# Performance work log

Measured on AMD Instinct MI355X. Metric: run time of the kernel, lower is better.

The kernel has to match this reference:

```python
import jax, jax.numpy as jnp
import numpy as np

N_NODES = 100000
N_EDGES = 1600000
IN_DIM, HID_DIM, OUT_DIM = 128, 64, 64


def setup_inputs() -> dict:
    key = jax.random.key(0)
    ks = jax.random.split(key, 8)
    x = jax.random.normal(ks[0], (N_NODES, IN_DIM), dtype=jnp.float32)
    edge_index = jax.random.randint(ks[1], (2, N_EDGES), 0, N_NODES, dtype=jnp.int32)
    edge_weight = jax.random.uniform(ks[2], (N_EDGES,), dtype=jnp.float32)
    # GCNConv parameters (glorot-ish init)
    w1 = jax.random.normal(ks[3], (IN_DIM, HID_DIM), dtype=jnp.float32) / np.sqrt(IN_DIM)
    b1 = jnp.zeros((HID_DIM,), dtype=jnp.float32)
    w2 = jax.random.normal(ks[4], (HID_DIM, OUT_DIM), dtype=jnp.float32) / np.sqrt(HID_DIM)
    b2 = jnp.zeros((OUT_DIM,), dtype=jnp.float32)
    return {"x": x, "edge_index": edge_index, "edge_weight": edge_weight,
            "w1": w1, "b1": b1, "w2": w2, "b2": b2}


def _gcn_conv(h, src, dst, edge_weight, w, b, n_nodes):
    # GCNConv(normalize=False): linear transform, then edge-weighted scatter-add
    # (source_to_target flow: gather from src, scatter-sum into dst), then bias.
    h = h @ w                                   # [N, out]
    msg = h[src] * edge_weight[:, None]          # [E, out] irregular gather
    agg = jax.ops.segment_sum(msg, dst, num_segments=n_nodes)  # [N, out]
    return agg + b


def reference(x, edge_index, edge_weight, w1, b1, w2, b2):
    src, dst = edge_index[0], edge_index[1]
    n = x.shape[0]
    # Dropout is identity in eval mode (training=False).
    h = _gcn_conv(x, src, dst, edge_weight, w1, b1, n)
    h = jax.nn.relu(h)
    out = _gcn_conv(h, src, dst, edge_weight, w2, b2, n)
    return out
```

## Files before the change

### kernel.cpp

```cpp
#include <hip/hip_runtime.h>
#include <hip/hip_bf16.h>


#define N_NODES 100000
#define N_EDGES 1600000
#define NB1     391
#define T1      3072
#define NT1     521
#define CAP1    4706
#define GB1     782

typedef unsigned short ushort_t;
typedef unsigned int uint_t;
typedef __attribute__((ext_vector_type(8))) short bf16x8;
typedef __attribute__((ext_vector_type(4))) float floatx4;
typedef __attribute__((ext_vector_type(8))) ushort_t ushort8v;

static __device__ __forceinline__ float bf2f(ushort_t h) {
    return __uint_as_float(((uint_t)h) << 16);
}
static __device__ __forceinline__ ushort_t f2bf(float f) {
    uint_t u = __float_as_uint(f);
    u = (u + 0x7FFF + ((u >> 16) & 1)) >> 16;
    return (ushort_t)u;
}

__global__ __launch_bounds__(512) void k_init(int* __restrict__ gcursor)
{
    int t = threadIdx.x;
    if (t < NB1) gcursor[t] = t * CAP1;
}

__global__ __launch_bounds__(512) void k_p1g1(
    const int* __restrict__ src, const int* __restrict__ dst,
    const float* __restrict__ ew, int* __restrict__ gcursor,
    int2* __restrict__ recs1, int E,
    const float* __restrict__ X, const float* __restrict__ W,
    ushort_t* __restrict__ Y, int N)
{
    __shared__ __align__(16) char smem[37056];
    const int tid = threadIdx.x;

    if (blockIdx.x < NT1) {
        int* cnt     = (int*)smem;
        int* start   = cnt + NB1;
        int* cursor  = start + NB1;
        int* gb      = cursor + NB1;
        int* wsum    = (int*)(smem + 6256);
        int* wexc    = wsum + 8;
        int2* stg    = (int2*)(smem + 6336);
        ushort_t* sb = (ushort_t*)(smem + 30912);
        const int t = tid, b = blockIdx.x;
        const int lane = t & 63, wv = t >> 6;

        if (t < NB1) cnt[t] = 0;
        __syncthreads();
        const int e0 = b * T1;
        const int e1 = min(E, e0 + T1);
        for (int e = e0 + t; e < e1; e += 512)
            atomicAdd(&cnt[dst[e] >> 8], 1);
        __syncthreads();

        const int v = (t < NB1) ? cnt[t] : 0;
        int x = v;
        #pragma unroll
        for (int off = 1; off < 64; off <<= 1) {
            int y = __shfl_up(x, off);
            if (lane >= off) x += y;
        }
        if (lane == 63) wsum[wv] = x;
        __syncthreads();
        if (t < 8) {
            int w  = wsum[t];
            int xx = w;
            #pragma unroll
            for (int off = 1; off < 8; off <<= 1) {
                int y = __shfl_up(xx, off);
                if (t >= off) xx += y;
            }
            wexc[t] = xx - w;
        }
        __syncthreads();
        if (t < NB1) {
            int st = x + wexc[wv] - v;
            start[t]  = st;
            cursor[t] = st;
            gb[t]     = atomicAdd(&gcursor[t], v);
        }
        __syncthreads();

        for (int e = e0 + t; e < e1; e += 512) {
            int d  = dst[e];
            int bk = d >> 8;
            int p  = atomicAdd(&cursor[bk], 1);
            int2 r;
            r.x = ((d & 255) << 17) | src[e];
            r.y = __float_as_int(ew[e]);
            stg[p] = r;
            sb[p]  = (ushort_t)bk;
        }
        __syncthreads();
        const int n = e1 - e0;
        for (int i = t; i < n; i += 512) {
            int bk = sb[i];
            recs1[gb[bk] + (i - start[bk])] = stg[i];
        }
    } else {
        ushort_t* sA = (ushort_t*)smem;
        ushort_t* sB = (ushort_t*)(smem + 18432);
        const int b    = blockIdx.x - NT1;
        const int row0 = b * 128;

        for (int i = tid; i < 128 * 16; i += 512) {
            int k = i >> 4, n4 = (i & 15) * 4;
            float4 v = *(const float4*)(W + (size_t)k * 64 + n4);
            sB[(n4 + 0) * 136 + k] = f2bf(v.x);
            sB[(n4 + 1) * 136 + k] = f2bf(v.y);
            sB[(n4 + 2) * 136 + k] = f2bf(v.z);
            sB[(n4 + 3) * 136 + k] = f2bf(v.w);
        }
        for (int i = tid; i < 128 * 16; i += 512) {
            int r = i >> 4, c4 = (i & 15) * 4;
            int rg = row0 + r; if (rg > N - 1) rg = N - 1;
            float4 v = *(const float4*)(X + (size_t)rg * 128 + c4);
            *(ushort4*)(sA + r * 72 + c4) =
                make_ushort4(f2bf(v.x), f2bf(v.y), f2bf(v.z), f2bf(v.w));
        }
        __syncthreads();

        const int wid = tid >> 6, lane = tid & 63;
        const int m = lane & 15, quad = lane >> 4;
        floatx4 acc[4] = {};

        #pragma unroll
        for (int ksl = 0; ksl < 2; ++ksl) {
            bf16x8 a = *(const bf16x8*)(sA + (wid * 16 + m) * 72 + ksl * 32 + quad * 8);
            #pragma unroll
            for (int nt = 0; nt < 4; ++nt) {
                bf16x8 bfr = *(const bf16x8*)(sB + (nt * 16 + m) * 136 + ksl * 32 + quad * 8);
                acc[nt] = __builtin_amdgcn_mfma_f32_16x16x32_bf16(a, bfr, acc[nt], 0, 0, 0);
            }
        }
        __syncthreads();
        for (int i = tid; i < 128 * 16; i += 512) {
            int r = i >> 4, c4 = (i & 15) * 4;
            int rg = row0 + r; if (rg > N - 1) rg = N - 1;
            float4 v = *(const float4*)(X + (size_t)rg * 128 + 64 + c4);
            *(ushort4*)(sA + r * 72 + c4) =
                make_ushort4(f2bf(v.x), f2bf(v.y), f2bf(v.z), f2bf(v.w));
        }
        __syncthreads();
        #pragma unroll
        for (int ksl = 0; ksl < 2; ++ksl) {
            bf16x8 a = *(const bf16x8*)(sA + (wid * 16 + m) * 72 + ksl * 32 + quad * 8);
            #pragma unroll
            for (int nt = 0; nt < 4; ++nt) {
                bf16x8 bfr = *(const bf16x8*)(sB + (nt * 16 + m) * 136 + 64 + ksl * 32 + quad * 8);
                acc[nt] = __builtin_amdgcn_mfma_f32_16x16x32_bf16(a, bfr, acc[nt], 0, 0, 0);
            }
        }
        __syncthreads();
        #pragma unroll
        for (int nt = 0; nt < 4; ++nt)
            #pragma unroll
            for (int r = 0; r < 4; ++r)
                sA[(wid * 16 + quad * 4 + r) * 72 + nt * 16 + m] = f2bf(acc[nt][r]);
        __syncthreads();
        for (int i = tid; i < 128 * 8; i += 512) {
            int rr = i >> 3, c8 = (i & 7) * 8;
            int rg = row0 + rr;
            if (rg < N)
                *(ushort8v*)(Y + (size_t)rg * 64 + c8) =
                    *(const ushort8v*)(sA + rr * 72 + c8);
        }
    }
}

__global__ __launch_bounds__(1024) void k_pass2(
    const int2* __restrict__ recs1, const int* __restrict__ gcursor,
    int2* __restrict__ recs2, int2* __restrict__ nodeinfo, int N)
{
    __shared__ int cnt[256];
    __shared__ int s[256];
    __shared__ int cursor[256];
    const int t = threadIdx.x, b = blockIdx.x;
    const int lo = b * CAP1;
    const int hi = gcursor[b];

    if (t < 256) cnt[t] = 0;
    __syncthreads();
    for (int j = lo + t; j < hi; j += 1024)
        atomicAdd(&cnt[((uint_t)recs1[j].x) >> 17], 1);
    __syncthreads();
    const int v = (t < 256) ? cnt[t] : 0;
    if (t < 256) s[t] = v;
    #pragma unroll
    for (int off = 1; off < 256; off <<= 1) {
        __syncthreads();
        int a = (t >= off && t < 256) ? s[t - off] : 0;
        __syncthreads();
        if (t < 256) s[t] += a;
    }
    __syncthreads();
    if (t < 256) {
        const int stl = s[t] - v;
        cursor[t] = stl;
        const int ng = b * 256 + t;
        if (ng < N) {
            int2 ni; ni.x = lo + stl; ni.y = v;
            nodeinfo[ng] = ni;
        }
    }
    __syncthreads();
    for (int j = lo + t; j < hi; j += 1024) {
        int2 r = recs1[j];
        int dl = ((uint_t)r.x) >> 17;
        int p  = atomicAdd(&cursor[dl], 1);
        int2 o;
        o.x = r.x & 0x1FFFF;
        o.y = r.y;
        recs2[lo + p] = o;
    }
}

__global__ __launch_bounds__(256) void k_gemm2(
    const ushort_t* __restrict__ X, const float* __restrict__ W,
    ushort_t* __restrict__ Y, int N)
{
    __shared__ ushort_t sA[64 * 72];
    __shared__ ushort_t sB[64 * 72];
    const int tid  = threadIdx.x;
    const int row0 = blockIdx.x * 64;

    for (int i = tid; i < 64 * 16; i += 256) {
        int r = i >> 4, c4 = (i & 15) * 4;
        int rg = row0 + r; if (rg > N - 1) rg = N - 1;
        *(ushort4*)(sA + r * 72 + c4) =
            *(const ushort4*)(X + (size_t)rg * 64 + c4);
    }
    for (int i = tid; i < 64 * 16; i += 256) {
        int k = i >> 4, n4 = (i & 15) * 4;
        float4 v = *(const float4*)(W + (size_t)k * 64 + n4);
        sB[(n4 + 0) * 72 + k] = f2bf(v.x);
        sB[(n4 + 1) * 72 + k] = f2bf(v.y);
        sB[(n4 + 2) * 72 + k] = f2bf(v.z);
        sB[(n4 + 3) * 72 + k] = f2bf(v.w);
    }
    __syncthreads();

    const int wid = tid >> 6, lane = tid & 63;
    const int m = lane & 15, quad = lane >> 4;
    floatx4 acc[4] = {};

    #pragma unroll
    for (int ks = 0; ks < 2; ++ks) {
        bf16x8 a = *(const bf16x8*)(sA + (wid * 16 + m) * 72 + ks * 32 + quad * 8);
        #pragma unroll
        for (int nt = 0; nt < 4; ++nt) {
            bf16x8 bfr = *(const bf16x8*)(sB + (nt * 16 + m) * 72 + ks * 32 + quad * 8);
            acc[nt] = __builtin_amdgcn_mfma_f32_16x16x32_bf16(a, bfr, acc[nt], 0, 0, 0);
        }
    }
    __syncthreads();
    #pragma unroll
    for (int nt = 0; nt < 4; ++nt)
        #pragma unroll
        for (int r = 0; r < 4; ++r)
            sA[(wid * 16 + quad * 4 + r) * 72 + nt * 16 + m] = f2bf(acc[nt][r]);
    __syncthreads();
    for (int i = tid; i < 64 * 8; i += 256) {
        int rr = i >> 3, c8 = (i & 7) * 8;
        int rg = row0 + rr;
        if (rg < N)
            *(ushort8v*)(Y + (size_t)rg * 64 + c8) =
                *(const ushort8v*)(sA + rr * 72 + c8);
    }
}

template<bool RELU, bool OUT_BF16>
__global__ __launch_bounds__(256) void k_gather(
    const ushort_t* __restrict__ H, const int2* __restrict__ recs,
    const int2* __restrict__ nodeinfo, const float* __restrict__ bias,
    void* __restrict__ out)
{
    const int wid  = threadIdx.x >> 6;
    const int lane = threadIdx.x & 63;
    const int n0   = (blockIdx.x * 4 + wid) * 2;
    const int n1   = n0 + 1;

    const int2 niA = nodeinfo[n0];
    const int2 niB = nodeinfo[n1];
    int baseA = niA.x; const int endA = niA.x + niA.y;
    int baseB = niB.x; const int endB = niB.x + niB.y;

    const int g  = lane >> 4;
    const int c4 = (lane & 15) * 4;

    float a0 = 0.f, a1 = 0.f, a2 = 0.f, a3 = 0.f;
    float b0 = 0.f, b1 = 0.f, b2 = 0.f, b3 = 0.f;

    while (baseA < endA || baseB < endB) {
        int mA = endA - baseA; if (mA > 64) mA = 64;
        int mB = endB - baseB; if (mB > 64) mB = 64;
        int2 rA = (mA > 0) ? recs[baseA + (lane < mA ? lane : mA - 1)]
                           : make_int2(0, 0);
        int2 rB = (mB > 0) ? recs[baseB + (lane < mB ? lane : mB - 1)]
                           : make_int2(0, 0);
        float wAf = __int_as_float(rA.y);
        float wBf = __int_as_float(rB.y);
        int mm = mA > mB ? mA : mB;
        #pragma unroll 4
        for (int jj = 0; jj < mm; jj += 4) {
            int idx = jj + g;
            int   sA = __shfl(rA.x, idx);
            float wA = __shfl(wAf, idx);
            int   sB = __shfl(rB.x, idx);
            float wB = __shfl(wBf, idx);
            if (idx >= mA) wA = 0.f;
            if (idx >= mB) wB = 0.f;
            ushort4 hA = *(const ushort4*)(H + (size_t)sA * 64 + c4);
            ushort4 hB = *(const ushort4*)(H + (size_t)sB * 64 + c4);
            a0 = fmaf(wA, bf2f(hA.x), a0);
            a1 = fmaf(wA, bf2f(hA.y), a1);
            a2 = fmaf(wA, bf2f(hA.z), a2);
            a3 = fmaf(wA, bf2f(hA.w), a3);
            b0 = fmaf(wB, bf2f(hB.x), b0);
            b1 = fmaf(wB, bf2f(hB.y), b1);
            b2 = fmaf(wB, bf2f(hB.z), b2);
            b3 = fmaf(wB, bf2f(hB.w), b3);
        }
        baseA += 64;
        baseB += 64;
    }
    a0 += __shfl_down(a0, 32); a1 += __shfl_down(a1, 32);
    a2 += __shfl_down(a2, 32); a3 += __shfl_down(a3, 32);
    b0 += __shfl_down(b0, 32); b1 += __shfl_down(b1, 32);
    b2 += __shfl_down(b2, 32); b3 += __shfl_down(b3, 32);
    a0 += __shfl_down(a0, 16); a1 += __shfl_down(a1, 16);
    a2 += __shfl_down(a2, 16); a3 += __shfl_down(a3, 16);
    b0 += __shfl_down(b0, 16); b1 += __shfl_down(b1, 16);
    b2 += __shfl_down(b2, 16); b3 += __shfl_down(b3, 16);

    if (lane < 16) {
        float4 bv = *(const float4*)(bias + c4);
        float vA0 = a0 + bv.x, vA1 = a1 + bv.y, vA2 = a2 + bv.z, vA3 = a3 + bv.w;
        float vB0 = b0 + bv.x, vB1 = b1 + bv.y, vB2 = b2 + bv.z, vB3 = b3 + bv.w;
        if (RELU) {
            vA0 = fmaxf(vA0, 0.f); vA1 = fmaxf(vA1, 0.f);
            vA2 = fmaxf(vA2, 0.f); vA3 = fmaxf(vA3, 0.f);
            vB0 = fmaxf(vB0, 0.f); vB1 = fmaxf(vB1, 0.f);
            vB2 = fmaxf(vB2, 0.f); vB3 = fmaxf(vB3, 0.f);
        }
        if (OUT_BF16) {
            *(ushort4*)((ushort_t*)out + (size_t)n0 * 64 + c4) =
                make_ushort4(f2bf(vA0), f2bf(vA1), f2bf(vA2), f2bf(vA3));
            *(ushort4*)((ushort_t*)out + (size_t)n1 * 64 + c4) =
                make_ushort4(f2bf(vB0), f2bf(vB1), f2bf(vB2), f2bf(vB3));
        } else {
            *(float4*)((float*)out + (size_t)n0 * 64 + c4) =
                make_float4(vA0, vA1, vA2, vA3);
            *(float4*)((float*)out + (size_t)n1 * 64 + c4) =
                make_float4(vB0, vB1, vB2, vB3);
        }
    }
}

extern "C" void kernel_launch(void* const* d_in, const int* in_sizes, int n_in,
                              void* d_out, int out_size, void* d_ws, size_t ws_size,
                              hipStream_t stream) {
    const float* x   = (const float*)d_in[0];
    const int*   ei  = (const int*)  d_in[1];
    const float* ew  = (const float*)d_in[2];
    const float* w1  = (const float*)d_in[3];
    const float* b1  = (const float*)d_in[4];
    const float* w2  = (const float*)d_in[5];
    const float* b2  = (const float*)d_in[6];
    float* out = (float*)d_out;

    const int N = N_NODES, E = N_EDGES;
    const int* src = ei;
    const int* dst = ei + E;

    char* p = (char*)d_ws;
    ushort_t* bufA   = (ushort_t*)p;  p += (size_t)N_NODES * 64 * 2;
    int2*     recs2  = (int2*)p;      p += (size_t)NB1 * CAP1 * 8;
    int2*     recs1  = (int2*)p;
    ushort_t* bufB   = (ushort_t*)p;  p += (size_t)NB1 * CAP1 * 8;
    int*      gcur   = (int*)p;       p += 2048;
    int2*     ninfo  = (int2*)p;      p += (size_t)N_NODES * 8;

    k_init <<<1, 512, 0, stream>>>(gcur);
    k_p1g1 <<<NT1 + GB1, 512, 0, stream>>>(src, dst, ew, gcur, recs1, E,
                                           x, w1, bufA, N);
    k_pass2<<<NB1, 1024, 0, stream>>>(recs1, gcur, recs2, ninfo, N);

    k_gather<true, true><<<N / 8, 256, 0, stream>>>(bufA, recs2, ninfo, b1, bufB);

    k_gemm2<<<(N + 63) / 64, 256, 0, stream>>>(bufB, w2, bufA, N);
    k_gather<false, false><<<N / 8, 256, 0, stream>>>(bufA, recs2, ninfo, b2, out);
}
```

Measured before the change: 235.6 us.

## Fuse layer-1 gather with second GEMM; register-cache edges in partition pass

Merges the first aggregation kernel with the W2 matrix multiply so each wave aggregates two nodes and immediately multiplies them by W2 via MFMA, removing the intermediate write/read and one launch. The partition kernel now loads each thread's edges once into registers with larger tiles instead of reading dst twice. Costs: every small block re-converts W2 into shared memory, MFMA tiles are mostly padding, and shared memory use grows.

```diff
diff --git a/kernel.cpp b/kernel.cpp
--- a/kernel.cpp
+++ b/kernel.cpp
@@ -5,8 +5,9 @@
 #define N_NODES 100000
 #define N_EDGES 1600000
 #define NB1     391
-#define T1      3072
-#define NT1     521
+#define T1      4096
+#define NT1     391
+#define EPT     8
 #define CAP1    4706
 #define GB1     782
 
@@ -38,7 +39,7 @@
     const float* __restrict__ X, const float* __restrict__ W,
     ushort_t* __restrict__ Y, int N)
 {
-    __shared__ __align__(16) char smem[37056];
+    __shared__ __align__(16) char smem[47296];
     const int tid = threadIdx.x;
 
     if (blockIdx.x < NT1) {
@@ -49,16 +50,28 @@
         int* wsum    = (int*)(smem + 6256);
         int* wexc    = wsum + 8;
         int2* stg    = (int2*)(smem + 6336);
-        ushort_t* sb = (ushort_t*)(smem + 30912);
+        ushort_t* sb = (ushort_t*)(smem + 39104);
         const int t = tid, b = blockIdx.x;
         const int lane = t & 63, wv = t >> 6;
 
-        if (t < NB1) cnt[t] = 0;
-        __syncthreads();
+        int   rd[EPT]; int rs[EPT]; float rw[EPT];
         const int e0 = b * T1;
         const int e1 = min(E, e0 + T1);
-        for (int e = e0 + t; e < e1; e += 512)
-            atomicAdd(&cnt[dst[e] >> 8], 1);
+        #pragma unroll
+        for (int i = 0; i < EPT; ++i) {
+            int e  = e0 + t + i * 512;
+            int ee = (e < e1) ? e : e0;
+            rd[i] = dst[ee];
+            rs[i] = src[ee];
+            rw[i] = ew[ee];
+            if (e >= e1) rd[i] = -1;
+        }
+
+        if (t < NB1) cnt[t] = 0;
+        __syncthreads();
+        #pragma unroll
+        for (int i = 0; i < EPT; ++i)
+            if (rd[i] >= 0) atomicAdd(&cnt[rd[i] >> 8], 1);
         __syncthreads();
 
         const int v = (t < NB1) ? cnt[t] : 0;
@@ -89,15 +102,18 @@
         }
         __syncthreads();
 
-        for (int e = e0 + t; e < e1; e += 512) {
-            int d  = dst[e];
-            int bk = d >> 8;
-            int p  = atomicAdd(&cursor[bk], 1);
-            int2 r;
-            r.x = ((d & 255) << 17) | src[e];
-            r.y = __float_as_int(ew[e]);
-            stg[p] = r;
-            sb[p]  = (ushort_t)bk;
+        #pragma unroll
+        for (int i = 0; i < EPT; ++i) {
+            int d = rd[i];
+            if (d >= 0) {
+                int bk = d >> 8;
+                int p  = atomicAdd(&cursor[bk], 1);
+                int2 r;
+                r.x = ((d & 255) << 17) | rs[i];
+                r.y = __float_as_int(rw[i]);
+                stg[p] = r;
+                sb[p]  = (ushort_t)bk;
+            }
         }
         __syncthreads();
         const int n = e1 - e0;
@@ -223,70 +239,28 @@
     }
 }
 
-__global__ __launch_bounds__(256) void k_gemm2(
-    const ushort_t* __restrict__ X, const float* __restrict__ W,
-    ushort_t* __restrict__ Y, int N)
+__global__ __launch_bounds__(256) void k_gather_mm(
+    const ushort_t* __restrict__ H, const int2* __restrict__ recs,
+    const int2* __restrict__ nodeinfo, const float* __restrict__ bias1,
+    const float* __restrict__ W2, ushort_t* __restrict__ out)
 {
-    __shared__ ushort_t sA[64 * 72];
-    __shared__ ushort_t sB[64 * 72];
+    __shared__ ushort_t sW[64 * 72];
+    __shared__ ushort_t strip[4][128];
+
     const int tid  = threadIdx.x;
-    const int row0 = blockIdx.x * 64;
-
-    for (int i = tid; i < 64 * 16; i += 256) {
-        int r = i >> 4, c4 = (i & 15) * 4;
-        int rg = row0 + r; if (rg > N - 1) rg = N - 1;
-        *(ushort4*)(sA + r * 72 + c4) =
-            *(const ushort4*)(X + (size_t)rg * 64 + c4);
-    }
+    const int wid  = tid >> 6;
+    const int lane = tid & 63;
+    const int n0   = (blockIdx.x * 4 + wid) * 2;
+    const int n1   = n0 + 1;
+
     for (int i = tid; i < 64 * 16; i += 256) {
         int k = i >> 4, n4 = (i & 15) * 4;
-        float4 v = *(const float4*)(W + (size_t)k * 64 + n4);
-        sB[(n4 + 0) * 72 + k] = f2bf(v.x);
-        sB[(n4 + 1) * 72 + k] = f2bf(v.y);
-        sB[(n4 + 2) * 72 + k] = f2bf(v.z);
-        sB[(n4 + 3) * 72 + k] = f2bf(v.w);
-    }
-    __syncthreads();
-
-    const int wid = tid >> 6, lane = tid & 63;
-    const int m = lane & 15, quad = lane >> 4;
-    floatx4 acc[4] = {};
-
-    #pragma unroll
-    for (int ks = 0; ks < 2; ++ks) {
-        bf16x8 a = *(const bf16x8*)(sA + (wid * 16 + m) * 72 + ks * 32 + quad * 8);
-        #pragma unroll
-        for (int nt = 0; nt < 4; ++nt) {
-            bf16x8 bfr = *(const bf16x8*)(sB + (nt * 16 + m) * 72 + ks * 32 + quad * 8);
-            acc[nt] = __builtin_amdgcn_mfma_f32_16x16x32_bf16(a, bfr, acc[nt], 0, 0, 0);
-        }
-    }
-    __syncthreads();
-    #pragma unroll
-    for (int nt = 0; nt < 4; ++nt)
-        #pragma unroll
-        for (int r = 0; r < 4; ++r)
-            sA[(wid * 16 + quad * 4 + r) * 72 + nt * 16 + m] = f2bf(acc[nt][r]);
-    __syncthreads();
-    for (int i = tid; i < 64 * 8; i += 256) {
-        int rr = i >> 3, c8 = (i & 7) * 8;
-        int rg = row0 + rr;
-        if (rg < N)
-            *(ushort8v*)(Y + (size_t)rg * 64 + c8) =
-                *(const ushort8v*)(sA + rr * 72 + c8);
-    }
-}
-
-template<bool RELU, bool OUT_BF16>
-__global__ __launch_bounds__(256) void k_gather(
-    const ushort_t* __restrict__ H, const int2* __restrict__ recs,
-    const int2* __restrict__ nodeinfo, const float* __restrict__ bias,
-    void* __restrict__ out)
-{
-    const int wid  = threadIdx.x >> 6;
-    const int lane = threadIdx.x & 63;
-    const int n0   = (blockIdx.x * 4 + wid) * 2;
-    const int n1   = n0 + 1;
+        float4 v = *(const float4*)(W2 + (size_t)k * 64 + n4);
+        sW[(n4 + 0) * 72 + k] = f2bf(v.x);
+        sW[(n4 + 1) * 72 + k] = f2bf(v.y);
+        sW[(n4 + 2) * 72 + k] = f2bf(v.z);
+        sW[(n4 + 3) * 72 + k] = f2bf(v.w);
+    }
 
     const int2 niA = nodeinfo[n0];
     const int2 niB = nodeinfo[n1];
@@ -312,14 +286,14 @@
         #pragma unroll 4
         for (int jj = 0; jj < mm; jj += 4) {
             int idx = jj + g;
-            int   sA = __shfl(rA.x, idx);
-            float wA = __shfl(wAf, idx);
-            int   sB = __shfl(rB.x, idx);
-            float wB = __shfl(wBf, idx);
+            int   sA_ = __shfl(rA.x, idx);
+            float wA  = __shfl(wAf, idx);
+            int   sB_ = __shfl(rB.x, idx);
+            float wB  = __shfl(wBf, idx);
             if (idx >= mA) wA = 0.f;
             if (idx >= mB) wB = 0.f;
-            ushort4 hA = *(const ushort4*)(H + (size_t)sA * 64 + c4);
-            ushort4 hB = *(const ushort4*)(H + (size_t)sB * 64 + c4);
+            ushort4 hA = *(const ushort4*)(H + (size_t)sA_ * 64 + c4);
+            ushort4 hB = *(const ushort4*)(H + (size_t)sB_ * 64 + c4);
             a0 = fmaf(wA, bf2f(hA.x), a0);
             a1 = fmaf(wA, bf2f(hA.y), a1);
             a2 = fmaf(wA, bf2f(hA.z), a2);
@@ -342,26 +316,114 @@
     b2 += __shfl_down(b2, 16); b3 += __shfl_down(b3, 16);
 
     if (lane < 16) {
+        float4 bv = *(const float4*)(bias1 + c4);
+        float vA0 = fmaxf(a0 + bv.x, 0.f), vA1 = fmaxf(a1 + bv.y, 0.f);
+        float vA2 = fmaxf(a2 + bv.z, 0.f), vA3 = fmaxf(a3 + bv.w, 0.f);
+        float vB0 = fmaxf(b0 + bv.x, 0.f), vB1 = fmaxf(b1 + bv.y, 0.f);
+        float vB2 = fmaxf(b2 + bv.z, 0.f), vB3 = fmaxf(b3 + bv.w, 0.f);
+        *(ushort4*)(&strip[wid][0 * 64 + c4]) =
+            make_ushort4(f2bf(vA0), f2bf(vA1), f2bf(vA2), f2bf(vA3));
+        *(ushort4*)(&strip[wid][1 * 64 + c4]) =
+            make_ushort4(f2bf(vB0), f2bf(vB1), f2bf(vB2), f2bf(vB3));
+    }
+    __syncthreads();
+
+    const int m = lane & 15, quad = lane >> 4;
+    const ushort_t* sp = strip[wid];
+    floatx4 acc2[4] = {};
+    #pragma unroll
+    for (int ks = 0; ks < 2; ++ks) {
+        bf16x8 a = *(const bf16x8*)(sp + (m & 1) * 64 + ks * 32 + quad * 8);
+        #pragma unroll
+        for (int nt = 0; nt < 4; ++nt) {
+            bf16x8 bfr = *(const bf16x8*)(sW + (nt * 16 + m) * 72 + ks * 32 + quad * 8);
+            acc2[nt] = __builtin_amdgcn_mfma_f32_16x16x32_bf16(a, bfr, acc2[nt], 0, 0, 0);
+        }
+    }
+    if (quad == 0) {
+        #pragma unroll
+        for (int nt = 0; nt < 4; ++nt) {
+            strip[wid][0 * 64 + nt * 16 + m] = f2bf(acc2[nt][0]);
+            strip[wid][1 * 64 + nt * 16 + m] = f2bf(acc2[nt][1]);
+        }
+    }
+    __syncthreads();
+    if (lane < 32) {
+        int rr = lane >> 4, mm2 = lane & 15;
+        *(ushort4*)(out + (size_t)(n0 + rr) * 64 + mm2 * 4) =
+            *(const ushort4*)(&strip[wid][rr * 64 + mm2 * 4]);
+    }
+}
+
+__global__ __launch_bounds__(256) void k_gather2(
+    const ushort_t* __restrict__ H, const int2* __restrict__ recs,
+    const int2* __restrict__ nodeinfo, const float* __restrict__ bias,
+    float* __restrict__ out)
+{
+    const int wid  = threadIdx.x >> 6;
+    const int lane = threadIdx.x & 63;
+    const int n0   = (blockIdx.x * 4 + wid) * 2;
+    const int n1   = n0 + 1;
+
+    const int2 niA = nodeinfo[n0];
+    const int2 niB = nodeinfo[n1];
+    int baseA = niA.x; const int endA = niA.x + niA.y;
+    int baseB = niB.x; const int endB = niB.x + niB.y;
+
+    const int g  = lane >> 4;
+    const int c4 = (lane & 15) * 4;
+
+    float a0 = 0.f, a1 = 0.f, a2 = 0.f, a3 = 0.f;
+    float b0 = 0.f, b1 = 0.f, b2 = 0.f, b3 = 0.f;
+
+    while (baseA < endA || baseB < endB) {
+        int mA = endA - baseA; if (mA > 64) mA = 64;
+        int mB = endB - baseB; if (mB > 64) mB = 64;
+        int2 rA = (mA > 0) ? recs[baseA + (lane < mA ? lane : mA - 1)]
+                           : make_int2(0, 0);
+        int2 rB = (mB > 0) ? recs[baseB + (lane < mB ? lane : mB - 1)]
+                           : make_int2(0, 0);
+        float wAf = __int_as_float(rA.y);
+        float wBf = __int_as_float(rB.y);
+        int mm = mA > mB ? mA : mB;
+        #pragma unroll 4
+        for (int jj = 0; jj < mm; jj += 4) {
+            int idx = jj + g;
+            int   sA_ = __shfl(rA.x, idx);
+            float wA  = __shfl(wAf, idx);
+            int   sB_ = __shfl(rB.x, idx);
+            float wB  = __shfl(wBf, idx);
+            if (idx >= mA) wA = 0.f;
+            if (idx >= mB) wB = 0.f;
+            ushort4 hA = *(const ushort4*)(H + (size_t)sA_ * 64 + c4);
+            ushort4 hB = *(const ushort4*)(H + (size_t)sB_ * 64 + c4);
+            a0 = fmaf(wA, bf2f(hA.x), a0);
+            a1 = fmaf(wA, bf2f(hA.y), a1);
+            a2 = fmaf(wA, bf2f(hA.z), a2);
+            a3 = fmaf(wA, bf2f(hA.w), a3);
+            b0 = fmaf(wB, bf2f(hB.x), b0);
+            b1 = fmaf(wB, bf2f(hB.y), b1);
+            b2 = fmaf(wB, bf2f(hB.z), b2);
+            b3 = fmaf(wB, bf2f(hB.w), b3);
+        }
+        baseA += 64;
+        baseB += 64;
+    }
+    a0 += __shfl_down(a0, 32); a1 += __shfl_down(a1, 32);
+    a2 += __shfl_down(a2, 32); a3 += __shfl_down(a3, 32);
+    b0 += __shfl_down(b0, 32); b1 += __shfl_down(b1, 32);
+    b2 += __shfl_down(b2, 32); b3 += __shfl_down(b3, 32);
+    a0 += __shfl_down(a0, 16); a1 += __shfl_down(a1, 16);
+    a2 += __shfl_down(a2, 16); a3 += __shfl_down(a3, 16);
+    b0 += __shfl_down(b0, 16); b1 += __shfl_down(b1, 16);
+    b2 += __shfl_down(b2, 16); b3 += __shfl_down(b3, 16);
+
+    if (lane < 16) {
         float4 bv = *(const float4*)(bias + c4);
-        float vA0 = a0 + bv.x, vA1 = a1 + bv.y, vA2 = a2 + bv.z, vA3 = a3 + bv.w;
-        float vB0 = b0 + bv.x, vB1 = b1 + bv.y, vB2 = b2 + bv.z, vB3 = b3 + bv.w;
-        if (RELU) {
-            vA0 = fmaxf(vA0, 0.f); vA1 = fmaxf(vA1, 0.f);
-            vA2 = fmaxf(vA2, 0.f); vA3 = fmaxf(vA3, 0.f);
-            vB0 = fmaxf(vB0, 0.f); vB1 = fmaxf(vB1, 0.f);
-            vB2 = fmaxf(vB2, 0.f); vB3 = fmaxf(vB3, 0.f);
-        }
-        if (OUT_BF16) {
-            *(ushort4*)((ushort_t*)out + (size_t)n0 * 64 + c4) =
-                make_ushort4(f2bf(vA0), f2bf(vA1), f2bf(vA2), f2bf(vA3));
-            *(ushort4*)((ushort_t*)out + (size_t)n1 * 64 + c4) =
-                make_ushort4(f2bf(vB0), f2bf(vB1), f2bf(vB2), f2bf(vB3));
-        } else {
-            *(float4*)((float*)out + (size_t)n0 * 64 + c4) =
-                make_float4(vA0, vA1, vA2, vA3);
-            *(float4*)((float*)out + (size_t)n1 * 64 + c4) =
-                make_float4(vB0, vB1, vB2, vB3);
-        }
+        *(float4*)(out + (size_t)n0 * 64 + c4) =
+            make_float4(a0 + bv.x, a1 + bv.y, a2 + bv.z, a3 + bv.w);
+        *(float4*)(out + (size_t)n1 * 64 + c4) =
+            make_float4(b0 + bv.x, b1 + bv.y, b2 + bv.z, b3 + bv.w);
     }
 }
 
@@ -394,8 +456,7 @@
                                            x, w1, bufA, N);
     k_pass2<<<NB1, 1024, 0, stream>>>(recs1, gcur, recs2, ninfo, N);
 
-    k_gather<true, true><<<N / 8, 256, 0, stream>>>(bufA, recs2, ninfo, b1, bufB);
-
-    k_gemm2<<<(N + 63) / 64, 256, 0, stream>>>(bufB, w2, bufA, N);
-    k_gather<false, false><<<N / 8, 256, 0, stream>>>(bufA, recs2, ninfo, b2, out);
-}
+    k_gather_mm<<<N / 8, 256, 0, stream>>>(bufA, recs2, ninfo, b1, w2, bufB);
+
+    k_gather2<<<N / 8, 256, 0, stream>>>(bufB, recs2, ninfo, b2, out);
+}
```

Result: slower. 247.8 us (+5.2%).
